# Optimization experiments

Measured on AMD Instinct MI355X. Metric: run time of the kernel, lower is better.

The kernel has to match this reference:

```python
import jax, jax.numpy as jnp
import numpy as np

RADIUS = 0.5
NEG_INF = -jnp.inf


def setup_inputs() -> dict:
    key = jax.random.key(0)
    ks = jax.random.split(key, 10)
    N_q, N_o, pos_dim, latent_dim = 2048, 2048, 3, 64
    enc_dim = 3 * pos_dim  # q_pos, o_pos, rel
    inp = {
        "h_obs": jax.random.normal(ks[0], (N_o, latent_dim), dtype=jnp.float32),
        "x_obs": jax.random.normal(ks[1], (N_o, latent_dim), dtype=jnp.float32),
        "pos_obs": jax.random.uniform(ks[2], (N_o, pos_dim), dtype=jnp.float32),
        "pos_query": jax.random.uniform(ks[3], (N_q, pos_dim), dtype=jnp.float32),
        # kernel_mlp: Linear(enc_dim->latent) + ReLU + Linear(latent->1)
        "W1": jax.random.normal(ks[4], (enc_dim, latent_dim), dtype=jnp.float32) / np.sqrt(enc_dim),
        "b1": jnp.zeros((latent_dim,), dtype=jnp.float32),
        "W2": jax.random.normal(ks[5], (latent_dim, 1), dtype=jnp.float32) / np.sqrt(latent_dim),
        "b2": jnp.zeros((1,), dtype=jnp.float32),
        # value_proj: Linear(latent->latent)
        "Wv": jax.random.normal(ks[6], (latent_dim, latent_dim), dtype=jnp.float32) / np.sqrt(latent_dim),
        "bv": jnp.zeros((latent_dim,), dtype=jnp.float32),
    }
    return inp


def reference(h_obs, x_obs, pos_obs, pos_query, W1, b1, W2, b2, Wv, bv):
    # rel: [N_q, N_o, pos_dim]
    rel = pos_query[:, None, :] - pos_obs[None, :, :]
    N_q, N_o, _ = rel.shape
    pos_q_exp = jnp.broadcast_to(pos_query[:, None, :], rel.shape)
    pos_o_exp = jnp.broadcast_to(pos_obs[None, :, :], rel.shape)
    kernel_input = jnp.concatenate([pos_q_exp, pos_o_exp, rel], axis=-1)  # [N_q, N_o, 3*pos_dim]
    # small pointwise MLP over all pairs
    hidden = jax.nn.relu(jnp.einsum('qoe,el->qol', kernel_input, W1) + b1)  # [N_q, N_o, latent]
    logits = jnp.einsum('qol,lk->qok', hidden, W2)[..., 0] + b2[0]          # [N_q, N_o]
    # radius mask
    dist = jnp.linalg.norm(rel, axis=-1)
    logits = jnp.where(dist > RADIUS, NEG_INF, logits)
    # softmax over observations (dim=1)
    weights = jax.nn.softmax(logits, axis=1)  # [N_q, N_o]
    v = h_obs @ Wv + bv                        # [N_o, latent]
    h_query = weights @ v                      # [N_q, latent]
    return h_query
```

## Files before the change

### kernel.cpp

```cpp
#include <hip/hip_runtime.h>

#define NQ 2048
#define NO 2048
#define NOC 32

constexpr size_t OFF_PH = 0;
constexpr size_t OFF_PS = (size_t)NOC * NQ * 64;

__global__ __launch_bounds__(256, 4) void gano_main(
    const float* __restrict__ h_obs,
    const float* __restrict__ pos_obs,
    const float* __restrict__ pos_query,
    const float* __restrict__ W1,
    const float* __restrict__ b1,
    const float* __restrict__ W2,
    float* __restrict__ Ph,
    float* __restrict__ Ps)
{
    __shared__ __align__(16) float tl[64 * 68];
    __shared__ __align__(16) float ue[16 * 64 * 4];
    __shared__ float w1q[3 * 64];
    __shared__ float w1o[3 * 64];
    __shared__ float b1l[64];
    __shared__ __align__(16) float w2l[64];
    __shared__ float po[3 * 64];
    __shared__ float sbuf[4 * 64];

    const int tid  = threadIdx.x;
    const int lane = tid & 63;
    const int wave = __builtin_amdgcn_readfirstlane(tid >> 6);
    const int qg = blockIdx.x >> 5;
    const int oc = blockIdx.x & 31;
    const int obase = oc * 64;
    const int q = qg * 64 + lane;

    if (tid < 64) {
        float w6 = W1[6 * 64 + tid], w7 = W1[7 * 64 + tid], w8 = W1[8 * 64 + tid];
        w1q[0 * 64 + tid] = W1[0 * 64 + tid] + w6;
        w1q[1 * 64 + tid] = W1[1 * 64 + tid] + w7;
        w1q[2 * 64 + tid] = W1[2 * 64 + tid] + w8;
        w1o[0 * 64 + tid] = W1[3 * 64 + tid] - w6;
        w1o[1 * 64 + tid] = W1[4 * 64 + tid] - w7;
        w1o[2 * 64 + tid] = W1[5 * 64 + tid] - w8;
        b1l[tid] = b1[tid];
        w2l[tid] = W2[tid];
    }
    float pq0 = pos_query[q * 3 + 0];
    float pq1 = pos_query[q * 3 + 1];
    float pq2 = pos_query[q * 3 + 2];
    float po0 = pos_obs[(obase + lane) * 3 + 0];
    float po1 = pos_obs[(obase + lane) * 3 + 1];
    float po2 = pos_obs[(obase + lane) * 3 + 2];
    if (wave == 0) { po[lane] = po0; po[64 + lane] = po1; po[128 + lane] = po2; }
    __syncthreads();

#pragma unroll
    for (int j = 0; j < 16; ++j) {
        int l = wave * 16 + j;
        tl[l * 68 + lane] = po0 * w1o[l] + po1 * w1o[64 + l] + po2 * w1o[128 + l];
    }
#pragma unroll
    for (int k = 0; k < 4; ++k) {
        int lb = wave * 4 + k;
        float4 uv;
        {
            int l = lb * 4;
            uv.x = b1l[l+0] + pq0 * w1q[l+0] + pq1 * w1q[64 + l+0] + pq2 * w1q[128 + l+0];
            uv.y = b1l[l+1] + pq0 * w1q[l+1] + pq1 * w1q[64 + l+1] + pq2 * w1q[128 + l+1];
            uv.z = b1l[l+2] + pq0 * w1q[l+2] + pq1 * w1q[64 + l+2] + pq2 * w1q[128 + l+2];
            uv.w = b1l[l+3] + pq0 * w1q[l+3] + pq1 * w1q[64 + l+3] + pq2 * w1q[128 + l+3];
        }
        *(float4*)(ue + (size_t)(lb * 64 + lane) * 4) = uv;
    }
    __syncthreads();

    float lg[16];
#pragma unroll
    for (int o = 0; o < 16; ++o) lg[o] = 0.f;
    const int ow = wave * 16;
#pragma unroll
    for (int lb = 0; lb < 16; ++lb) {
        float4 u4 = *(const float4*)(ue + (size_t)(lb * 64 + lane) * 4);
        float4 w4 = *(const float4*)(w2l + lb * 4);
#pragma unroll
        for (int dl = 0; dl < 4; ++dl) {
            const int l = lb * 4 + dl;
            const float4* tr = (const float4*)(tl + l * 68 + ow);
            float ul = (dl == 0) ? u4.x : (dl == 1) ? u4.y : (dl == 2) ? u4.z : u4.w;
            float wl = (dl == 0) ? w4.x : (dl == 1) ? w4.y : (dl == 2) ? w4.z : w4.w;
#pragma unroll
            for (int j = 0; j < 4; ++j) {
                float4 t4 = tr[j];
                lg[4 * j + 0] += wl * fmaxf(ul + t4.x, 0.f);
                lg[4 * j + 1] += wl * fmaxf(ul + t4.y, 0.f);
                lg[4 * j + 2] += wl * fmaxf(ul + t4.z, 0.f);
                lg[4 * j + 3] += wl * fmaxf(ul + t4.w, 0.f);
            }
        }
    }
    float e[16], spart = 0.f;
#pragma unroll
    for (int o = 0; o < 16; ++o) {
        float d0 = pq0 - po[ow + o];
        float d1 = pq1 - po[64 + ow + o];
        float d2 = pq2 - po[128 + ow + o];
        float dd = d0 * d0 + d1 * d1 + d2 * d2;
        float ev = (dd > 0.25f) ? 0.f : __expf(lg[o]);
        e[o] = ev; spart += ev;
    }
    __syncthreads();
#pragma unroll
    for (int o = 0; o < 16; ++o) ue[(size_t)(ow + o) * 64 + lane] = e[o];
    sbuf[wave * 64 + lane] = spart;
    __syncthreads();

    float h0 = 0.f, h1 = 0.f, h2 = 0.f, h3 = 0.f, h4 = 0.f, h5 = 0.f, h6 = 0.f, h7 = 0.f;
    float h8 = 0.f, h9 = 0.f, hA = 0.f, hB = 0.f, hC = 0.f, hD = 0.f, hE = 0.f, hF = 0.f;
    const float* vb = h_obs + (size_t)obase * 64 + ow;
#pragma unroll 4
    for (int o = 0; o < 64; ++o) {
        float eo = ue[(size_t)o * 64 + lane];
        const float4* vr = (const float4*)(vb + (size_t)o * 64);
        float4 v0 = vr[0], v1 = vr[1], v2 = vr[2], v3 = vr[3];
        h0 += eo * v0.x; h1 += eo * v0.y; h2 += eo * v0.z; h3 += eo * v0.w;
        h4 += eo * v1.x; h5 += eo * v1.y; h6 += eo * v1.z; h7 += eo * v1.w;
        h8 += eo * v2.x; h9 += eo * v2.y; hA += eo * v2.z; hB += eo * v2.w;
        hC += eo * v3.x; hD += eo * v3.y; hE += eo * v3.z; hF += eo * v3.w;
    }

    float* hp = Ph + ((size_t)oc * NQ + (size_t)qg * 64 + lane) * 64 + ow;
    ((float4*)hp)[0] = make_float4(h0, h1, h2, h3);
    ((float4*)hp)[1] = make_float4(h4, h5, h6, h7);
    ((float4*)hp)[2] = make_float4(h8, h9, hA, hB);
    ((float4*)hp)[3] = make_float4(hC, hD, hE, hF);
    if (wave == 0) {
        float s = sbuf[lane] + sbuf[64 + lane] + sbuf[128 + lane] + sbuf[192 + lane];
        Ps[(size_t)oc * NQ + (size_t)qg * 64 + lane] = s;
    }
}

__global__ __launch_bounds__(256, 2) void gano_comb(
    const float* __restrict__ Ph,
    const float* __restrict__ Ps,
    const float* __restrict__ Wv,
    const float* __restrict__ bv,
    float* __restrict__ out)
{
    __shared__ __align__(16) float wv[64 * 64];
    __shared__ __align__(16) float g[4 * 68];
    const int tid  = threadIdx.x;
    const int lane = tid & 63;
    const int wave = tid >> 6;
    const int q0 = blockIdx.x * 4;
    {
        const float4* src = (const float4*)Wv;
        float4* dst = (float4*)wv;
#pragma unroll
        for (int k = 0; k < 4; ++k) dst[tid + k * 256] = src[tid + k * 256];
    }
    {
        const int qi = wave, k = lane;
        float acc = 0.f;
#pragma unroll
        for (int c = 0; c < NOC; ++c)
            acc += Ph[((size_t)c * NQ + q0 + qi) * 64 + k];
        g[qi * 68 + k] = acc;
        if (k == 0) {
            float ss = 0.f;
#pragma unroll
            for (int c = 0; c < NOC; ++c) ss += Ps[(size_t)c * NQ + q0 + qi];
            g[qi * 68 + 64] = ss;
        }
    }
    __syncthreads();
    const float* gq = g + wave * 68;
    float inv = 1.0f / gq[64];
    float a0 = 0.f, a1 = 0.f, a2 = 0.f, a3 = 0.f;
#pragma unroll
    for (int kb = 0; kb < 16; ++kb) {
        float4 g4 = *(const float4*)(gq + kb * 4);
        a0 += g4.x * wv[(kb * 4 + 0) * 64 + lane];
        a1 += g4.y * wv[(kb * 4 + 1) * 64 + lane];
        a2 += g4.z * wv[(kb * 4 + 2) * 64 + lane];
        a3 += g4.w * wv[(kb * 4 + 3) * 64 + lane];
    }
    out[(size_t)(q0 + wave) * 64 + lane] = ((a0 + a1) + (a2 + a3)) * inv + bv[lane];
}

extern "C" void kernel_launch(void* const* d_in, const int* in_sizes, int n_in,
                              void* d_out, int out_size, void* d_ws, size_t ws_size,
                              hipStream_t stream) {
    const float* h_obs     = (const float*)d_in[0];
    const float* pos_obs   = (const float*)d_in[2];
    const float* pos_query = (const float*)d_in[3];
    const float* W1        = (const float*)d_in[4];
    const float* b1        = (const float*)d_in[5];
    const float* W2        = (const float*)d_in[6];
    const float* Wv        = (const float*)d_in[8];
    const float* bv        = (const float*)d_in[9];
    float* ws  = (float*)d_ws;
    float* out = (float*)d_out;

    gano_main<<<dim3(1024), dim3(256), 0, stream>>>(h_obs, pos_obs, pos_query, W1, b1, W2,
                                                    ws + OFF_PH, ws + OFF_PS);
    gano_comb<<<dim3(NQ / 4), dim3(256), 0, stream>>>(ws + OFF_PH, ws + OFF_PS, Wv, bv, out);
}
```

Measured before the change: 107.8 us.

## Compute pairwise MLP hidden layer in packed fp16 with fdot2 accumulation

Converts the per-observation and per-query hidden-layer terms to packed half2 values stored in shared memory. The ReLU is then evaluated with packed fp16 add/max, and the W2 reduction uses fdot2 into fp32 accumulators. This roughly halves the VALU instruction count and LDS traffic of the dominant pairwise loop. The cost is reduced precision in the hidden activations and logits, which feed exp and may drift from the fp32 reference.

```diff
diff --git a/kernel.cpp b/kernel.cpp
--- a/kernel.cpp
+++ b/kernel.cpp
@@ -6,6 +6,27 @@
 
 constexpr size_t OFF_PH = 0;
 constexpr size_t OFF_PS = (size_t)NOC * NQ * 64;
+
+typedef _Float16 h2t __attribute__((ext_vector_type(2)));
+
+#if defined(__has_builtin)
+#if __has_builtin(__builtin_amdgcn_fdot2)
+#define FDOT2(a, b, c) __builtin_amdgcn_fdot2((a), (b), (c), false)
+#endif
+#endif
+#ifndef FDOT2
+#define FDOT2(a, b, c) ((c) + (float)(a)[0] * (float)(b)[0] + (float)(a)[1] * (float)(b)[1])
+#endif
+
+__device__ __forceinline__ float pack2(float a, float b) {
+    return __builtin_bit_cast(float, __builtin_amdgcn_cvt_pkrtz(a, b));
+}
+__device__ __forceinline__ h2t ash2(float f) {
+    return __builtin_bit_cast(h2t, f);
+}
+__device__ __forceinline__ h2t relu2(h2t x) {
+    return __builtin_elementwise_max(x, (h2t)(_Float16)0);
+}
 
 __global__ __launch_bounds__(256, 4) void gano_main(
     const float* __restrict__ h_obs,
@@ -17,12 +38,12 @@
     float* __restrict__ Ph,
     float* __restrict__ Ps)
 {
-    __shared__ __align__(16) float tl[64 * 68];
-    __shared__ __align__(16) float ue[16 * 64 * 4];
+    __shared__ __align__(16) float tl2[8 * 64 * 4];
+    __shared__ __align__(16) float ue[64 * 64];
     __shared__ float w1q[3 * 64];
     __shared__ float w1o[3 * 64];
     __shared__ float b1l[64];
-    __shared__ __align__(16) float w2l[64];
+    __shared__ __align__(16) float w2h[32];
     __shared__ float po[3 * 64];
     __shared__ float sbuf[4 * 64];
 
@@ -43,7 +64,10 @@
         w1o[1 * 64 + tid] = W1[4 * 64 + tid] - w7;
         w1o[2 * 64 + tid] = W1[5 * 64 + tid] - w8;
         b1l[tid] = b1[tid];
-        w2l[tid] = W2[tid];
+    }
+    if (tid >= 64 && tid < 96) {
+        int p = tid - 64;
+        w2h[p] = pack2(W2[2 * p], W2[2 * p + 1]);
     }
     float pq0 = pos_query[q * 3 + 0];
     float pq1 = pos_query[q * 3 + 1];
@@ -54,23 +78,34 @@
     if (wave == 0) { po[lane] = po0; po[64 + lane] = po1; po[128 + lane] = po2; }
     __syncthreads();
 
-#pragma unroll
-    for (int j = 0; j < 16; ++j) {
-        int l = wave * 16 + j;
-        tl[l * 68 + lane] = po0 * w1o[l] + po1 * w1o[64 + l] + po2 * w1o[128 + l];
-    }
-#pragma unroll
-    for (int k = 0; k < 4; ++k) {
-        int lb = wave * 4 + k;
-        float4 uv;
-        {
-            int l = lb * 4;
-            uv.x = b1l[l+0] + pq0 * w1q[l+0] + pq1 * w1q[64 + l+0] + pq2 * w1q[128 + l+0];
-            uv.y = b1l[l+1] + pq0 * w1q[l+1] + pq1 * w1q[64 + l+1] + pq2 * w1q[128 + l+1];
-            uv.z = b1l[l+2] + pq0 * w1q[l+2] + pq1 * w1q[64 + l+2] + pq2 * w1q[128 + l+2];
-            uv.w = b1l[l+3] + pq0 * w1q[l+3] + pq1 * w1q[64 + l+3] + pq2 * w1q[128 + l+3];
-        }
-        *(float4*)(ue + (size_t)(lb * 64 + lane) * 4) = uv;
+    {
+        float tv[16];
+#pragma unroll
+        for (int j = 0; j < 16; ++j) {
+            int l = wave * 16 + j;
+            tv[j] = po0 * w1o[l] + po1 * w1o[64 + l] + po2 * w1o[128 + l];
+        }
+        float4 p0, p1;
+        p0.x = pack2(tv[0], tv[1]);  p0.y = pack2(tv[2], tv[3]);
+        p0.z = pack2(tv[4], tv[5]);  p0.w = pack2(tv[6], tv[7]);
+        p1.x = pack2(tv[8], tv[9]);  p1.y = pack2(tv[10], tv[11]);
+        p1.z = pack2(tv[12], tv[13]); p1.w = pack2(tv[14], tv[15]);
+        *(float4*)(tl2 + (size_t)((2 * wave) * 64 + lane) * 4) = p0;
+        *(float4*)(tl2 + (size_t)((2 * wave + 1) * 64 + lane) * 4) = p1;
+    }
+#pragma unroll
+    for (int k = 0; k < 2; ++k) {
+        const int c = wave * 2 + k;
+        float uv[8];
+#pragma unroll
+        for (int d = 0; d < 8; ++d) {
+            int l = c * 8 + d;
+            uv[d] = b1l[l] + pq0 * w1q[l] + pq1 * w1q[64 + l] + pq2 * w1q[128 + l];
+        }
+        float4 up;
+        up.x = pack2(uv[0], uv[1]); up.y = pack2(uv[2], uv[3]);
+        up.z = pack2(uv[4], uv[5]); up.w = pack2(uv[6], uv[7]);
+        *(float4*)(ue + (size_t)(c * 64 + lane) * 4) = up;
     }
     __syncthreads();
 
@@ -79,23 +114,25 @@
     for (int o = 0; o < 16; ++o) lg[o] = 0.f;
     const int ow = wave * 16;
 #pragma unroll
-    for (int lb = 0; lb < 16; ++lb) {
-        float4 u4 = *(const float4*)(ue + (size_t)(lb * 64 + lane) * 4);
-        float4 w4 = *(const float4*)(w2l + lb * 4);
-#pragma unroll
-        for (int dl = 0; dl < 4; ++dl) {
-            const int l = lb * 4 + dl;
-            const float4* tr = (const float4*)(tl + l * 68 + ow);
-            float ul = (dl == 0) ? u4.x : (dl == 1) ? u4.y : (dl == 2) ? u4.z : u4.w;
-            float wl = (dl == 0) ? w4.x : (dl == 1) ? w4.y : (dl == 2) ? w4.z : w4.w;
-#pragma unroll
-            for (int j = 0; j < 4; ++j) {
-                float4 t4 = tr[j];
-                lg[4 * j + 0] += wl * fmaxf(ul + t4.x, 0.f);
-                lg[4 * j + 1] += wl * fmaxf(ul + t4.y, 0.f);
-                lg[4 * j + 2] += wl * fmaxf(ul + t4.z, 0.f);
-                lg[4 * j + 3] += wl * fmaxf(ul + t4.w, 0.f);
-            }
+    for (int c = 0; c < 8; ++c) {
+        float4 u4 = *(const float4*)(ue + (size_t)(c * 64 + lane) * 4);
+        float4 w4 = *(const float4*)(w2h + c * 4);
+        h2t u0 = ash2(u4.x), u1 = ash2(u4.y), u2 = ash2(u4.z), u3 = ash2(u4.w);
+        h2t w0 = ash2(w4.x), w1 = ash2(w4.y), w2 = ash2(w4.z), w3 = ash2(w4.w);
+        const float4* tr = (const float4*)tl2 + (c * 64 + ow);
+#pragma unroll
+        for (int j = 0; j < 16; ++j) {
+            float4 t4 = tr[j];
+            h2t a0 = relu2(u0 + ash2(t4.x));
+            h2t a1 = relu2(u1 + ash2(t4.y));
+            h2t a2 = relu2(u2 + ash2(t4.z));
+            h2t a3 = relu2(u3 + ash2(t4.w));
+            float acc = lg[j];
+            acc = FDOT2(a0, w0, acc);
+            acc = FDOT2(a1, w1, acc);
+            acc = FDOT2(a2, w2, acc);
+            acc = FDOT2(a3, w3, acc);
+            lg[j] = acc;
         }
     }
     float e[16], spart = 0.f;
```

Measured after the change: 104.6 us. 1.03x faster.
